# Kernel optimization log

Hardware: AMD Instinct MI355X
Metric: run time of the kernel (lower is better)

## Reference

```python
import jax, jax.numpy as jnp
import numpy as np

N_HEADS = 8
D_EMBED = 512
D_CROSS = 768
D_HEAD = D_EMBED // N_HEADS


def setup_inputs() -> dict:
    key = jax.random.key(0)
    ks = jax.random.split(key, 12)
    B, SQ, SKV = 8, 4096, 77
    s_e = 1.0 / np.sqrt(D_EMBED)
    s_c = 1.0 / np.sqrt(D_CROSS)
    return {
        "latent": jax.random.normal(ks[0], (B, SQ, D_EMBED), jnp.float32),
        "context": jax.random.normal(ks[1], (B, SKV, D_CROSS), jnp.float32),
        "wq": jax.random.normal(ks[2], (D_EMBED, D_EMBED), jnp.float32) * s_e,
        "bq": jax.random.normal(ks[3], (D_EMBED,), jnp.float32) * 0.01,
        "wk": jax.random.normal(ks[4], (D_CROSS, D_EMBED), jnp.float32) * s_c,
        "bk": jax.random.normal(ks[5], (D_EMBED,), jnp.float32) * 0.01,
        "wv": jax.random.normal(ks[6], (D_CROSS, D_EMBED), jnp.float32) * s_c,
        "bv": jax.random.normal(ks[7], (D_EMBED,), jnp.float32) * 0.01,
        "wo": jax.random.normal(ks[8], (D_EMBED, D_EMBED), jnp.float32) * s_e,
        "bo": jax.random.normal(ks[9], (D_EMBED,), jnp.float32) * 0.01,
    }


def reference(latent, context, wq, bq, wk, bk, wv, bv, wo, bo):
    B, SQ, _ = latent.shape
    SKV = context.shape[1]
    # projections; weights stored as (in, out)
    q = latent @ wq + bq                     # [B, SQ, D_EMBED]
    k = context @ wk + bk                    # [B, SKV, D_EMBED]
    v = context @ wv + bv                    # [B, SKV, D_EMBED]
    # split heads -> [B, H, S, Dh]
    q = q.reshape(B, SQ, N_HEADS, D_HEAD).transpose(0, 2, 1, 3)
    k = k.reshape(B, SKV, N_HEADS, D_HEAD).transpose(0, 2, 1, 3)
    v = v.reshape(B, SKV, N_HEADS, D_HEAD).transpose(0, 2, 1, 3)
    scale = 1.0 / np.sqrt(D_HEAD).astype(np.float32)
    w = jnp.einsum("bhqd,bhkd->bhqk", q, k) * scale  # [B, H, SQ, SKV]
    w = jax.nn.softmax(w, axis=-1)
    out = jnp.einsum("bhqk,bhkd->bhqd", w, v)        # [B, H, SQ, Dh]
    out = out.transpose(0, 2, 1, 3).reshape(B, SQ, D_EMBED)
    return out @ wo + bo
```

## Files before the change

kernel.cpp:

```cpp
#include <hip/hip_runtime.h>


typedef __attribute__((ext_vector_type(8))) __bf16 bf16x8;
typedef __attribute__((ext_vector_type(4))) float f32x4;

#define DEVI static __device__ __forceinline__

typedef __attribute__((address_space(3))) void lds_void_t;
typedef const __attribute__((address_space(1))) void gbl_void_t;
#define GLDS16(gsrc, ldst) \
  __builtin_amdgcn_global_load_lds((gbl_void_t*)(gsrc), (lds_void_t*)(ldst), 16, 0, 0)

DEVI unsigned short f2bf(float f) {
  unsigned int u = __float_as_uint(f);
  u += 0x7FFFu + ((u >> 16) & 1u);
  return (unsigned short)(u >> 16);
}

DEVI unsigned int pack2bf(float a, float b) {
  return (unsigned int)f2bf(a) | ((unsigned int)f2bf(b) << 16);
}

__global__ __launch_bounds__(256) void cvt_bf16_kernel(const float* __restrict__ in,
                                                       unsigned int* __restrict__ out4) {
  size_t i = (size_t)blockIdx.x * 256 + threadIdx.x;
  const float4* in4 = (const float4*)in;
  float4 a = in4[2 * i];
  float4 b = in4[2 * i + 1];
  uint4 o;
  o.x = pack2bf(a.x, a.y);
  o.y = pack2bf(a.z, a.w);
  o.z = pack2bf(b.x, b.y);
  o.w = pack2bf(b.z, b.w);
  *(uint4*)(out4 + 4 * i) = o;
}

__global__ __launch_bounds__(256) void wtrans_all_kernel(
    const float* __restrict__ wq, const float* __restrict__ wk,
    const float* __restrict__ wv, const float* __restrict__ wo,
    unsigned short* __restrict__ wqT, unsigned short* __restrict__ wkT,
    unsigned short* __restrict__ wvT, unsigned short* __restrict__ woT) {
  __shared__ float tile[32][33];
  int bid = blockIdx.x;
  int tid = threadIdx.x;
  const float* in;
  unsigned short* out;
  int K, r;
  if (bid < 256)       { in = wq; out = wqT; K = 512; r = bid; }
  else if (bid < 640)  { in = wk; out = wkT; K = 768; r = bid - 256; }
  else if (bid < 1024) { in = wv; out = wvT; K = 768; r = bid - 640; }
  else                 { in = wo; out = woT; K = 512; r = bid - 1024; }
  int n0 = (r & 15) * 32, k0 = (r >> 4) * 32;
  int tx = tid & 31, ty = tid >> 5;
#pragma unroll
  for (int j = 0; j < 4; ++j)
    tile[ty * 4 + j][tx] = in[(size_t)(k0 + ty * 4 + j) * 512 + n0 + tx];
  __syncthreads();
#pragma unroll
  for (int j = 0; j < 4; ++j)
    out[(size_t)(n0 + ty * 4 + j) * K + k0 + tx] = f2bf(tile[tx][ty * 4 + j]);
}

__global__ __launch_bounds__(256) void kv_proj_kernel(const float* __restrict__ ctx,
                                                      const unsigned short* __restrict__ wkT,
                                                      const unsigned short* __restrict__ wvT,
                                                      const float* __restrict__ bk,
                                                      const float* __restrict__ bv,
                                                      unsigned short* __restrict__ Kp,
                                                      unsigned short* __restrict__ Vt) {
  __shared__ __align__(16) unsigned short As[64][40];
  __shared__ __align__(16) unsigned short Bs[64][40];
  int bid = blockIdx.x;
  int sel = bid / 80;
  int rem = bid % 80;
  int mt = rem / 8, nt = rem % 8;
  const unsigned short* wT = sel ? wvT : wkT;
  const float* bias = sel ? bv : bk;
  int tid = threadIdx.x;
  int l = tid & 63, w = tid >> 6;
  int lr = l & 15, lg = l >> 4;

  f32x4 acc[4] = {};
  for (int k0 = 0; k0 < 768; k0 += 32) {
#pragma unroll
    for (int it = 0; it < 2; ++it) {
      int idx4 = it * 256 + tid;
      int r = idx4 >> 3, q4 = idx4 & 7;
      int m = mt * 64 + r;
      float4 v = {0.f, 0.f, 0.f, 0.f};
      if (m < 616) v = *(const float4*)(ctx + (size_t)m * 768 + k0 + q4 * 4);
      ushort4 o;
      o.x = f2bf(v.x); o.y = f2bf(v.y); o.z = f2bf(v.z); o.w = f2bf(v.w);
      *(ushort4*)&As[r][q4 * 4] = o;
    }
    {
      int c = tid >> 2, q8 = tid & 3;
      *(uint4*)&Bs[c][q8 * 8] =
          *(const uint4*)(wT + (size_t)(nt * 64 + c) * 768 + k0 + q8 * 8);
    }
    __syncthreads();
    bf16x8 a = *(const bf16x8*)&As[w * 16 + lr][lg * 8];
#pragma unroll
    for (int n = 0; n < 4; ++n) {
      bf16x8 bb = *(const bf16x8*)&Bs[n * 16 + lr][lg * 8];
      acc[n] = __builtin_amdgcn_mfma_f32_16x16x32_bf16(a, bb, acc[n], 0, 0, 0);
    }
    __syncthreads();
  }
#pragma unroll
  for (int n = 0; n < 4; ++n) {
#pragma unroll
    for (int reg = 0; reg < 4; ++reg) {
      int m = mt * 64 + w * 16 + lg * 4 + reg;
      if (m < 616) {
        int bI = m / 77, s = m % 77;
        int col = nt * 64 + n * 16 + lr;
        int h = col >> 6, d = col & 63;
        float v = acc[n][reg] + bias[col];
        if (sel == 0)
          Kp[(((size_t)(bI * 8 + h)) * 80 + s) * 64 + d] = f2bf(v);
        else
          Vt[(((size_t)(bI * 8 + h)) * 64 + d) * 96 + s] = f2bf(v);
      }
    }
  }
}

#define KSTEP(t, boff)                                                        \
  {                                                                           \
    if ((t) < 15)                                                             \
      asm volatile("s_waitcnt vmcnt(4)" ::: "memory");                        \
    else                                                                      \
      asm volatile("s_waitcnt vmcnt(0)" ::: "memory");                        \
    __builtin_amdgcn_s_barrier();                                             \
    __builtin_amdgcn_sched_barrier(0);                                        \
    const unsigned short* bufA = smem + (boff);                               \
    const unsigned short* bufB = bufA + 4096;                                 \
    const int swB = (lr >> 1) & 3;                                            \
    bf16x8 af[4], bv8[4];                                                     \
    _Pragma("unroll") for (int m = 0; m < 4; ++m)                             \
        af[m] = *(const bf16x8*)&bufA[(wr + m * 16 + lr) * 32 +               \
                                      (lg ^ swB) * 8];                        \
    _Pragma("unroll") for (int n = 0; n < 4; ++n)                             \
        bv8[n] = *(const bf16x8*)&bufB[(wc + n * 16 + lr) * 32 +              \
                                       (lg ^ swB) * 8];                       \
    asm volatile("s_waitcnt lgkmcnt(0)" ::: "memory");                        \
    __builtin_amdgcn_sched_barrier(0);                                        \
    __builtin_amdgcn_s_barrier();                                             \
    if ((t) <= 13) {                                                          \
      int nk = ((t) + 2) * 32;                                                \
      GLDS16(gA + nk, smem + (boff) + w * 1024);                              \
      GLDS16(gA + nk + 16 * 512, smem + (boff) + w * 1024 + 512);             \
      GLDS16(gB + nk, smem + (boff) + 4096 + w * 1024);                       \
      GLDS16(gB + nk + 16 * 512, smem + (boff) + 4096 + w * 1024 + 512);      \
    }                                                                         \
    _Pragma("unroll") for (int m = 0; m < 4; ++m)                             \
        _Pragma("unroll") for (int n = 0; n < 4; ++n)                         \
            acc[m][n] = __builtin_amdgcn_mfma_f32_16x16x32_bf16(              \
                af[m], bv8[n], acc[m][n], 0, 0, 0);                           \
  }

#define GEMM_PROLOGUE()                                                       \
  GLDS16(gA, smem + w * 1024);                                                \
  GLDS16(gA + 16 * 512, smem + w * 1024 + 512);                               \
  GLDS16(gB, smem + 4096 + w * 1024);                                         \
  GLDS16(gB + 16 * 512, smem + 4096 + w * 1024 + 512);                        \
  GLDS16(gA + 32, smem + 8192 + w * 1024);                                    \
  GLDS16(gA + 32 + 16 * 512, smem + 8192 + w * 1024 + 512);                   \
  GLDS16(gB + 32, smem + 12288 + w * 1024);                                   \
  GLDS16(gB + 32 + 16 * 512, smem + 12288 + w * 1024 + 512);

__global__ __launch_bounds__(256, 4) void qproj_attn_kernel(
    const unsigned short* __restrict__ A, const unsigned short* __restrict__ BT,
    const float* __restrict__ bias, const unsigned short* __restrict__ Kp,
    const unsigned short* __restrict__ Vt, unsigned short* __restrict__ Oq) {
  __shared__ __align__(16) unsigned short smem[18432];

  int bid = ((blockIdx.x & 7) << 7) | (blockIdx.x >> 3);
  size_t mbase = (size_t)(bid >> 2) * 128;
  int nbase = (bid & 3) * 128;
  int tid = threadIdx.x;
  int l = tid & 63, w = tid >> 6;
  int lr = l & 15, lg = l >> 4;
  int wr = (w >> 1) * 64, wc = (w & 1) * 64;

  const unsigned short* gA = A + (mbase + w * 32 + (l >> 2)) * 512 +
                             (((l & 3) ^ ((l >> 3) & 3))) * 8;
  const unsigned short* gB = BT + (size_t)(nbase + w * 32 + (l >> 2)) * 512 +
                             (((l & 3) ^ ((l >> 3) & 3))) * 8;

  GEMM_PROLOGUE();

  f32x4 acc[4][4] = {};
#pragma unroll 1
  for (int t = 0; t < 16; t += 2) {
    KSTEP(t, 0);
    KSTEP(t + 1, 8192);
  }

  unsigned short* Qme = smem + w * (64 * 72);
  float bb[4];
#pragma unroll
  for (int n = 0; n < 4; ++n) bb[n] = bias[nbase + wc + n * 16 + lr];
#pragma unroll
  for (int m = 0; m < 4; ++m)
#pragma unroll
    for (int n = 0; n < 4; ++n)
#pragma unroll
      for (int reg = 0; reg < 4; ++reg)
        Qme[(m * 16 + lg * 4 + reg) * 72 + n * 16 + lr] = f2bf(acc[m][n][reg] + bb[n]);

  bf16x8 qf[4][2];
#pragma unroll
  for (int rg = 0; rg < 4; ++rg) {
    qf[rg][0] = *(const bf16x8*)&Qme[(rg * 16 + lr) * 72 + lg * 8];
    qf[rg][1] = *(const bf16x8*)&Qme[(rg * 16 + lr) * 72 + 32 + lg * 8];
  }

  unsigned short* Pme = Qme;
  for (int z = l; z < 256; z += 64) Pme[(z >> 4) * 104 + 80 + (z & 15)] = 0;

  int b = (int)(mbase >> 12);
  int h = (bid & 3) * 2 + (w & 1);
  const unsigned short* Kph = Kp + (size_t)(b * 8 + h) * (80 * 64);
  const unsigned short* Vth = Vt + (size_t)(b * 8 + h) * (64 * 96);

  const float C = 0.125f * 1.44269504088896f;

  auto QK = [&](int rg, f32x4* s) {
#pragma unroll
    for (int t = 0; t < 5; ++t) {
      const unsigned short* kr = Kph + (t * 16 + lr) * 64 + lg * 8;
      bf16x8 k0 = *(const bf16x8*)kr;
      bf16x8 k1 = *(const bf16x8*)(kr + 32);
      s[t] = __builtin_amdgcn_mfma_f32_16x16x32_bf16(qf[rg][0], k0, s[t], 0, 0, 0);
      s[t] = __builtin_amdgcn_mfma_f32_16x16x32_bf16(qf[rg][1], k1, s[t], 0, 0, 0);
    }
    if (lr >= 13) {
      s[4][0] = -1e30f; s[4][1] = -1e30f; s[4][2] = -1e30f; s[4][3] = -1e30f;
    }
  };

  f32x4 sc[5] = {};
  QK(0, sc);
#pragma unroll
  for (int rg = 0; rg < 4; ++rg) {
    float mx[4];
#pragma unroll
    for (int r = 0; r < 4; ++r)
      mx[r] = fmaxf(fmaxf(fmaxf(sc[0][r], sc[1][r]), fmaxf(sc[2][r], sc[3][r])), sc[4][r]);
#pragma unroll
    for (int d = 1; d < 16; d <<= 1)
#pragma unroll
      for (int r = 0; r < 4; ++r) mx[r] = fmaxf(mx[r], __shfl_xor(mx[r], d, 64));
    float p[5][4];
#pragma unroll
    for (int t = 0; t < 5; ++t)
#pragma unroll
      for (int r = 0; r < 4; ++r) p[t][r] = exp2f((sc[t][r] - mx[r]) * C);
#pragma unroll
    for (int t = 0; t < 5; ++t)
#pragma unroll
      for (int r = 0; r < 4; ++r)
        Pme[(lg * 4 + r) * 104 + t * 16 + lr] = f2bf(p[t][r]);

    float sm[4];
#pragma unroll
    for (int r = 0; r < 4; ++r)
      sm[r] = p[0][r] + p[1][r] + p[2][r] + p[3][r] + p[4][r];
#pragma unroll
    for (int d = 1; d < 16; d <<= 1)
#pragma unroll
      for (int r = 0; r < 4; ++r) sm[r] += __shfl_xor(sm[r], d, 64);
    float rs[4];
#pragma unroll
    for (int r = 0; r < 4; ++r) rs[r] = 1.0f / sm[r];

    f32x4 sn[5] = {};
    if (rg < 3) QK(rg + 1, sn);

    bf16x8 ap[3];
#pragma unroll
    for (int c = 0; c < 3; ++c) ap[c] = *(const bf16x8*)&Pme[lr * 104 + c * 32 + lg * 8];
#pragma unroll
    for (int ct = 0; ct < 4; ++ct) {
      f32x4 o = {};
#pragma unroll
      for (int c = 0; c < 3; ++c) {
        bf16x8 vv = *(const bf16x8*)(Vth + (size_t)(ct * 16 + lr) * 96 + c * 32 + lg * 8);
        o = __builtin_amdgcn_mfma_f32_16x16x32_bf16(ap[c], vv, o, 0, 0, 0);
      }
#pragma unroll
      for (int reg = 0; reg < 4; ++reg)
        Oq[(mbase + wr + rg * 16 + lg * 4 + reg) * 512 + nbase + wc + ct * 16 + lr] =
            f2bf(o[reg] * rs[reg]);
    }
#pragma unroll
    for (int t = 0; t < 5; ++t) sc[t] = sn[t];
  }
}

__global__ __launch_bounds__(256) void gemm512_glds_kernel(
    const unsigned short* __restrict__ A, const unsigned short* __restrict__ BT,
    const float* __restrict__ bias, float* __restrict__ Out) {
  __shared__ __align__(16) unsigned short smem[16384];
  int bid = ((blockIdx.x & 7) << 7) | (blockIdx.x >> 3);
  size_t mbase = (size_t)(bid >> 2) * 128;
  int nbase = (bid & 3) * 128;
  int tid = threadIdx.x;
  int l = tid & 63, w = tid >> 6;
  int lr = l & 15, lg = l >> 4;
  int wr = (w >> 1) * 64, wc = (w & 1) * 64;

  const unsigned short* gA = A + (mbase + w * 32 + (l >> 2)) * 512 +
                             (((l & 3) ^ ((l >> 3) & 3))) * 8;
  const unsigned short* gB = BT + (size_t)(nbase + w * 32 + (l >> 2)) * 512 +
                             (((l & 3) ^ ((l >> 3) & 3))) * 8;

  GEMM_PROLOGUE();

  f32x4 acc[4][4] = {};
#pragma unroll 1
  for (int t = 0; t < 16; t += 2) {
    KSTEP(t, 0);
    KSTEP(t + 1, 8192);
  }

#pragma unroll
  for (int m = 0; m < 4; ++m) {
#pragma unroll
    for (int n = 0; n < 4; ++n) {
#pragma unroll
      for (int reg = 0; reg < 4; ++reg) {
        size_t row = mbase + wr + m * 16 + lg * 4 + reg;
        int col = nbase + wc + n * 16 + lr;
        Out[row * 512 + col] = acc[m][n][reg] + bias[col];
      }
    }
  }
}

static const size_t OFF_Q   = 0;
static const size_t OFF_KP  = 33554432;
static const size_t OFF_VT  = OFF_KP + 655360;
static const size_t OFF_WQT = OFF_VT + 786432;
static const size_t OFF_WKT = OFF_WQT + 524288;
static const size_t OFF_WVT = OFF_WKT + 786432;
static const size_t OFF_WOT = OFF_WVT + 786432;
static const size_t WS_NEEDED = OFF_WOT + 524288;

extern "C" void kernel_launch(void* const* d_in, const int* in_sizes, int n_in,
                              void* d_out, int out_size, void* d_ws, size_t ws_size,
                              hipStream_t stream) {
  (void)in_sizes; (void)n_in; (void)out_size;
  if (ws_size < WS_NEEDED) return;

  const float* latent  = (const float*)d_in[0];
  const float* context = (const float*)d_in[1];
  const float* wq = (const float*)d_in[2];
  const float* bq = (const float*)d_in[3];
  const float* wk = (const float*)d_in[4];
  const float* bk = (const float*)d_in[5];
  const float* wv = (const float*)d_in[6];
  const float* bv = (const float*)d_in[7];
  const float* wo = (const float*)d_in[8];
  const float* bo = (const float*)d_in[9];
  float* out = (float*)d_out;

  char* ws = (char*)d_ws;
  unsigned short* wsQ = (unsigned short*)(ws + OFF_Q);
  unsigned short* Kp  = (unsigned short*)(ws + OFF_KP);
  unsigned short* Vt  = (unsigned short*)(ws + OFF_VT);
  unsigned short* wqT = (unsigned short*)(ws + OFF_WQT);
  unsigned short* wkT = (unsigned short*)(ws + OFF_WKT);
  unsigned short* wvT = (unsigned short*)(ws + OFF_WVT);
  unsigned short* woT = (unsigned short*)(ws + OFF_WOT);

  unsigned short* latBF = (unsigned short*)d_out;

  wtrans_all_kernel<<<1280, 256, 0, stream>>>(wq, wk, wv, wo,
                                              wqT, wkT, wvT, woT);
  hipMemsetAsync(ws + OFF_KP, 0, 655360 + 786432, stream);
  kv_proj_kernel<<<160, 256, 0, stream>>>(context, wkT, wvT, bk, bv, Kp, Vt);
  cvt_bf16_kernel<<<8192, 256, 0, stream>>>(latent, (unsigned int*)latBF);
  qproj_attn_kernel<<<1024, 256, 0, stream>>>(latBF, wqT, bq, Kp, Vt, wsQ);
  gemm512_glds_kernel<<<1024, 256, 0, stream>>>(wsQ, woT, bo, out);
}
```

Measured before the change: 124.6 us.

## Fuse prep kernels and keep softmax probabilities in registers via transposed QK MFMA

Merges the weight transpose, the workspace memset and the latent bf16 conversion into a single prep launch, which removes two launches and a memset. In the attention kernel the QK MFMA operands are swapped so that each lane holds one query row's scores. That turns the row max and sum into a few in-register reductions plus two cross-lane shuffles. The normalized probabilities are packed with v_cvt_pk_bf16 and redistributed to the PV A-operand layout with shuffles instead of an LDS round trip, and the invalid key columns are masked by zeroing probabilities instead of writing -1e30 scores. This adds many ds_bpermute shuffles and makes the correctness of the padding mask depend on the exact lane layout.

```diff
diff --git a/kernel.cpp b/kernel.cpp
--- a/kernel.cpp
+++ b/kernel.cpp
@@ -21,28 +21,40 @@
   return (unsigned int)f2bf(a) | ((unsigned int)f2bf(b) << 16);
 }
 
-__global__ __launch_bounds__(256) void cvt_bf16_kernel(const float* __restrict__ in,
-                                                       unsigned int* __restrict__ out4) {
-  size_t i = (size_t)blockIdx.x * 256 + threadIdx.x;
-  const float4* in4 = (const float4*)in;
-  float4 a = in4[2 * i];
-  float4 b = in4[2 * i + 1];
-  uint4 o;
-  o.x = pack2bf(a.x, a.y);
-  o.y = pack2bf(a.z, a.w);
-  o.z = pack2bf(b.x, b.y);
-  o.w = pack2bf(b.z, b.w);
-  *(uint4*)(out4 + 4 * i) = o;
-}
-
-__global__ __launch_bounds__(256) void wtrans_all_kernel(
+DEVI unsigned int cvt_pk_bf16(float lo, float hi) {
+  unsigned int r;
+  asm("v_cvt_pk_bf16_f32 %0, %1, %2" : "=v"(r) : "v"(lo), "v"(hi));
+  return r;
+}
+
+__global__ __launch_bounds__(256) void prep_kernel(
     const float* __restrict__ wq, const float* __restrict__ wk,
     const float* __restrict__ wv, const float* __restrict__ wo,
     unsigned short* __restrict__ wqT, unsigned short* __restrict__ wkT,
-    unsigned short* __restrict__ wvT, unsigned short* __restrict__ woT) {
-  __shared__ float tile[32][33];
+    unsigned short* __restrict__ wvT, unsigned short* __restrict__ woT,
+    uint4* __restrict__ zbuf, const float* __restrict__ latent,
+    unsigned int* __restrict__ latBF4) {
   int bid = blockIdx.x;
   int tid = threadIdx.x;
+  if (bid >= 1632) {
+    size_t i = (size_t)(bid - 1632) * 256 + tid;
+    const float4* in4 = (const float4*)latent;
+    float4 a = in4[2 * i];
+    float4 b = in4[2 * i + 1];
+    uint4 o;
+    o.x = pack2bf(a.x, a.y);
+    o.y = pack2bf(a.z, a.w);
+    o.z = pack2bf(b.x, b.y);
+    o.w = pack2bf(b.z, b.w);
+    *(uint4*)(latBF4 + 4 * i) = o;
+    return;
+  }
+  if (bid >= 1280) {
+    uint4 z = {0u, 0u, 0u, 0u};
+    zbuf[(size_t)(bid - 1280) * 256 + tid] = z;
+    return;
+  }
+  __shared__ float tile[32][33];
   const float* in;
   unsigned short* out;
   int K, r;
@@ -217,9 +229,6 @@
     qf[rg][1] = *(const bf16x8*)&Qme[(rg * 16 + lr) * 72 + 32 + lg * 8];
   }
 
-  unsigned short* Pme = Qme;
-  for (int z = l; z < 256; z += 64) Pme[(z >> 4) * 104 + 80 + (z & 15)] = 0;
-
   int b = (int)(mbase >> 12);
   int h = (bid & 3) * 2 + (w & 1);
   const unsigned short* Kph = Kp + (size_t)(b * 8 + h) * (80 * 64);
@@ -233,55 +242,72 @@
       const unsigned short* kr = Kph + (t * 16 + lr) * 64 + lg * 8;
       bf16x8 k0 = *(const bf16x8*)kr;
       bf16x8 k1 = *(const bf16x8*)(kr + 32);
-      s[t] = __builtin_amdgcn_mfma_f32_16x16x32_bf16(qf[rg][0], k0, s[t], 0, 0, 0);
-      s[t] = __builtin_amdgcn_mfma_f32_16x16x32_bf16(qf[rg][1], k1, s[t], 0, 0, 0);
-    }
-    if (lr >= 13) {
-      s[4][0] = -1e30f; s[4][1] = -1e30f; s[4][2] = -1e30f; s[4][3] = -1e30f;
+      s[t] = __builtin_amdgcn_mfma_f32_16x16x32_bf16(k0, qf[rg][0], s[t], 0, 0, 0);
+      s[t] = __builtin_amdgcn_mfma_f32_16x16x32_bf16(k1, qf[rg][1], s[t], 0, 0, 0);
     }
   };
+
+  const int srcLo = 32 * (lg & 1) + lr;
+  const int srcHi = srcLo + 16;
+  const int selHi = lg >> 1;
 
   f32x4 sc[5] = {};
   QK(0, sc);
 #pragma unroll
   for (int rg = 0; rg < 4; ++rg) {
-    float mx[4];
-#pragma unroll
-    for (int r = 0; r < 4; ++r)
-      mx[r] = fmaxf(fmaxf(fmaxf(sc[0][r], sc[1][r]), fmaxf(sc[2][r], sc[3][r])), sc[4][r]);
-#pragma unroll
-    for (int d = 1; d < 16; d <<= 1)
-#pragma unroll
-      for (int r = 0; r < 4; ++r) mx[r] = fmaxf(mx[r], __shfl_xor(mx[r], d, 64));
+    float mx = sc[0][0];
+#pragma unroll
+    for (int t = 0; t < 5; ++t)
+#pragma unroll
+      for (int r = 0; r < 4; ++r) mx = fmaxf(mx, sc[t][r]);
+    mx = fmaxf(mx, __shfl_xor(mx, 16, 64));
+    mx = fmaxf(mx, __shfl_xor(mx, 32, 64));
     float p[5][4];
 #pragma unroll
     for (int t = 0; t < 5; ++t)
 #pragma unroll
-      for (int r = 0; r < 4; ++r) p[t][r] = exp2f((sc[t][r] - mx[r]) * C);
+      for (int r = 0; r < 4; ++r) p[t][r] = exp2f((sc[t][r] - mx) * C);
+    if (lg == 3) { p[4][1] = 0.f; p[4][2] = 0.f; p[4][3] = 0.f; }
+    float sm = 0.f;
 #pragma unroll
     for (int t = 0; t < 5; ++t)
 #pragma unroll
-      for (int r = 0; r < 4; ++r)
-        Pme[(lg * 4 + r) * 104 + t * 16 + lr] = f2bf(p[t][r]);
-
-    float sm[4];
-#pragma unroll
-    for (int r = 0; r < 4; ++r)
-      sm[r] = p[0][r] + p[1][r] + p[2][r] + p[3][r] + p[4][r];
-#pragma unroll
-    for (int d = 1; d < 16; d <<= 1)
-#pragma unroll
-      for (int r = 0; r < 4; ++r) sm[r] += __shfl_xor(sm[r], d, 64);
-    float rs[4];
-#pragma unroll
-    for (int r = 0; r < 4; ++r) rs[r] = 1.0f / sm[r];
+      for (int r = 0; r < 4; ++r) sm += p[t][r];
+    sm += __shfl_xor(sm, 16, 64);
+    sm += __shfl_xor(sm, 32, 64);
+    float rs = 1.0f / sm;
+    unsigned int pk[5][2];
+#pragma unroll
+    for (int t = 0; t < 5; ++t) {
+      pk[t][0] = cvt_pk_bf16(p[t][0] * rs, p[t][1] * rs);
+      pk[t][1] = cvt_pk_bf16(p[t][2] * rs, p[t][3] * rs);
+    }
 
     f32x4 sn[5] = {};
     if (rg < 3) QK(rg + 1, sn);
 
     bf16x8 ap[3];
 #pragma unroll
-    for (int c = 0; c < 3; ++c) ap[c] = *(const bf16x8*)&Pme[lr * 104 + c * 32 + lg * 8];
+    for (int c = 0; c < 3; ++c) {
+      unsigned int a0 = __shfl((int)pk[2 * c][0], srcLo, 64);
+      unsigned int a1 = __shfl((int)pk[2 * c][1], srcLo, 64);
+      unsigned int a2 = __shfl((int)pk[2 * c][0], srcHi, 64);
+      unsigned int a3 = __shfl((int)pk[2 * c][1], srcHi, 64);
+      unsigned int b0 = 0, b1 = 0, b2 = 0, b3 = 0;
+      if (c < 2) {
+        b0 = __shfl((int)pk[2 * c + 1][0], srcLo, 64);
+        b1 = __shfl((int)pk[2 * c + 1][1], srcLo, 64);
+        b2 = __shfl((int)pk[2 * c + 1][0], srcHi, 64);
+        b3 = __shfl((int)pk[2 * c + 1][1], srcHi, 64);
+      }
+      uint4 u;
+      u.x = selHi ? b0 : a0;
+      u.y = selHi ? b1 : a1;
+      u.z = selHi ? b2 : a2;
+      u.w = selHi ? b3 : a3;
+      ap[c] = *(bf16x8*)&u;
+    }
+
 #pragma unroll
     for (int ct = 0; ct < 4; ++ct) {
       f32x4 o = {};
@@ -293,7 +319,7 @@
 #pragma unroll
       for (int reg = 0; reg < 4; ++reg)
         Oq[(mbase + wr + rg * 16 + lg * 4 + reg) * 512 + nbase + wc + ct * 16 + lr] =
-            f2bf(o[reg] * rs[reg]);
+            f2bf(o[reg]);
     }
 #pragma unroll
     for (int t = 0; t < 5; ++t) sc[t] = sn[t];
@@ -378,11 +404,10 @@
 
   unsigned short* latBF = (unsigned short*)d_out;
 
-  wtrans_all_kernel<<<1280, 256, 0, stream>>>(wq, wk, wv, wo,
-                                              wqT, wkT, wvT, woT);
-  hipMemsetAsync(ws + OFF_KP, 0, 655360 + 786432, stream);
+  prep_kernel<<<1280 + 352 + 8192, 256, 0, stream>>>(
+      wq, wk, wv, wo, wqT, wkT, wvT, woT, (uint4*)(ws + OFF_KP), latent,
+      (unsigned int*)latBF);
   kv_proj_kernel<<<160, 256, 0, stream>>>(context, wkT, wvT, bk, bv, Kp, Vt);
-  cvt_bf16_kernel<<<8192, 256, 0, stream>>>(latent, (unsigned int*)latBF);
   qproj_attn_kernel<<<1024, 256, 0, stream>>>(latBF, wqT, bq, Kp, Vt, wsQ);
   gemm512_glds_kernel<<<1024, 256, 0, stream>>>(wsQ, woT, bo, out);
 }
```

Measured after the change: 113.9 us. 8.6% less time.
